# Performance work log

Hardware: AMD Instinct MI355X
Metric: run time of the kernel (lower is better)

Reference implementation:

```python
import jax, jax.numpy as jnp
import numpy as np

N, E = 100000, 1600000
ENT, OCU, SAI, IJ = 64, 64, 64, 8


def setup_inputs() -> dict:
    key = jax.random.key(0)
    ks = jax.random.split(key, 14)

    def lin(k, fan_in, fan_out):
        s = 1.0 / np.sqrt(fan_in)
        kw, kb = jax.random.split(k)
        w = jax.random.uniform(kw, (fan_in, fan_out), minval=-s, maxval=s, dtype=jnp.float32)
        b = jax.random.uniform(kb, (fan_out,), minval=-s, maxval=s, dtype=jnp.float32)
        return w, b

    we_w1, we_b1 = lin(ks[0], 2 * ENT + 1 + IJ, OCU)
    we_w2, we_b2 = lin(ks[1], OCU, OCU)
    wx_w1, wx_b1 = lin(ks[2], OCU, OCU)
    wx_w2, wx_b2 = lin(ks[3], OCU, 1)
    wh_w1, wh_b1 = lin(ks[4], ENT + OCU, OCU)
    wh_w2, wh_b2 = lin(ks[5], OCU, SAI)
    wv_w1, wv_b1 = lin(ks[6], ENT, OCU)
    wv_w2, wv_b2 = lin(ks[7], OCU, 1)

    return {
        "h": jax.random.normal(ks[8], (N, ENT), dtype=jnp.float32),
        "x": jax.random.normal(ks[9], (N, 3), dtype=jnp.float32),
        "velocidade": jax.random.normal(ks[10], (N, 3), dtype=jnp.float32),
        "atributos_arestas": jax.random.normal(ks[11], (E, IJ), dtype=jnp.float32),
        "we_w1": we_w1, "we_b1": we_b1, "we_w2": we_w2, "we_b2": we_b2,
        "wx_w1": wx_w1, "wx_b1": wx_b1, "wx_w2": wx_w2, "wx_b2": wx_b2,
        "wh_w1": wh_w1, "wh_b1": wh_b1, "wh_w2": wh_w2, "wh_b2": wh_b2,
        "wv_w1": wv_w1, "wv_b1": wv_b1, "wv_w2": wv_w2, "wv_b2": wv_b2,
        "arestas": jax.random.randint(ks[12], (2, E), 0, N, dtype=jnp.int32),
    }


def reference(h, x, velocidade, atributos_arestas,
              we_w1, we_b1, we_w2, we_b2,
              wx_w1, wx_b1, wx_w2, wx_b2,
              wh_w1, wh_b1, wh_w2, wh_b2,
              wv_w1, wv_b1, wv_w2, wv_b2,
              arestas):
    linhas, cols = arestas[0], arestas[1]
    n = h.shape[0]

    # gather endpoint coordinates, radial distance per edge
    diferenca = x[linhas] - x[cols]                            # [E, 3]
    dif_radial = jnp.sum(diferenca * diferenca, axis=1, keepdims=True)  # [E, 1]

    # edge MLP phi_e on [h_i, h_j, ||x_i-x_j||^2, edge_attr]
    atributos = jnp.concatenate([h[linhas], h[cols], dif_radial, atributos_arestas], axis=1)
    m_ij = jnp.tanh(jnp.tanh(atributos @ we_w1 + we_b1) @ we_w2 + we_b2)   # [E, OCU]

    # phi_x: per-edge scalar gate on coordinate differences
    phi_x = jnp.tanh(jnp.tanh(m_ij @ wx_w1 + wx_b1) @ wx_w2 + wx_b2)       # [E, 1]

    # phi_v: per-node scalar gate on velocity
    phi_v = jnp.tanh(h @ wv_w1 + wv_b1) @ wv_w2 + wv_b2                    # [N, 1]

    # segment-mean of (diferenca * phi_x) over source nodes
    trans = diferenca * phi_x                                              # [E, 3]
    agg_sum = jax.ops.segment_sum(trans, linhas, num_segments=n)           # [N, 3]
    cnt = jax.ops.segment_sum(jnp.ones((E, 1), trans.dtype), linhas, num_segments=n)
    agg_mean = agg_sum / jnp.maximum(cnt, 1.0)

    velocidade_nova = velocidade * phi_v + agg_mean
    x_nova = x + velocidade_nova

    # segment-sum of edge messages, node update phi_h
    m_i = jax.ops.segment_sum(m_ij, linhas, num_segments=n)                # [N, OCU]
    h_cat = jnp.concatenate([h, m_i], axis=1)
    h_nova = jnp.tanh(h_cat @ wh_w1 + wh_b1) @ wh_w2 + wh_b2               # [N, SAI]

    return (h_nova, x_nova, velocidade_nova)
```

## Files before the change

### kernel.cpp

```cpp
#include <hip/hip_runtime.h>


typedef unsigned int uint;
typedef unsigned short u16;
typedef __attribute__((ext_vector_type(8))) short short8;
typedef __attribute__((ext_vector_type(4))) float f32x4;

#define UB_LO(u) __uint_as_float((u) << 16)
#define UB_HI(u) __uint_as_float((u) & 0xffff0000u)

__device__ __forceinline__ float fast_tanh(float x) {
    float e = __expf(2.0f * x);
    return 1.0f - 2.0f * __builtin_amdgcn_rcpf(e + 1.0f);
}
__device__ __forceinline__ u16 bf16rne(float f) {
    uint u = __float_as_uint(f);
    return (u16)((u + 0x7fffu + ((u >> 16) & 1u)) >> 16);
}
__device__ __forceinline__ uint packbf(float a, float b) {
    return (uint)bf16rne(a) | ((uint)bf16rne(b) << 16);
}
__device__ __forceinline__ uint packbf_fast(float a, float b) {
    return __builtin_amdgcn_perm(__float_as_uint(b), __float_as_uint(a), 0x07060302u);
}
__device__ __forceinline__ u16 trunc16(float f) {
    return (u16)(__float_as_uint(f) >> 16);
}
__device__ __forceinline__ int swzb(int b) { return b ^ ((b >> 3) & 0x70); }

__global__ void wprep_kernel(const float* __restrict__ we_w1, const float* __restrict__ we_w2,
                             const float* __restrict__ wx_w1, const float* __restrict__ wv_w1,
                             const float* __restrict__ wh_w1, const float* __restrict__ wh_w2,
                             u16* __restrict__ we1t, u16* __restrict__ we2t,
                             u16* __restrict__ wx1t, u16* __restrict__ wv1t,
                             u16* __restrict__ wh1t, u16* __restrict__ wh2t,
                             u16* __restrict__ wert) {
    int t = blockIdx.x * 256 + threadIdx.x;
    if (t < 8192) {
        int j = t >> 7, k = t & 127;
        we1t[t] = bf16rne(we_w1[k * 64 + j]);
        wh1t[t] = bf16rne(wh_w1[k * 64 + j]);
    }
    if (t < 4096) {
        int n = t >> 6, k = t & 63;
        we2t[t] = bf16rne(we_w2[k * 64 + n]);
        wx1t[t] = bf16rne(wx_w1[k * 64 + n]);
        wv1t[t] = bf16rne(wv_w1[k * 64 + n]);
        wh2t[t] = bf16rne(wh_w2[k * 64 + n]);
    }
    if (t < 2048) {
        int n = t >> 5, k = t & 31;
        float v = 0.0f;
        if (k == 0) v = we_w1[128 * 64 + n];
        else if (k <= 8) v = we_w1[(128 + k) * 64 + n];
        wert[t] = bf16rne(v);
    }
}

__global__ __launch_bounds__(256, 2)
void pre_mfma_kernel(const float* __restrict__ h, const float* __restrict__ we_b1,
                     const u16* __restrict__ we1t,
                     u16* __restrict__ HrB, u16* __restrict__ HcB, int N)
{
    __shared__ u16 X1[4096];
    __shared__ u16 X2[4096];
    const int tid = threadIdx.x, lane = tid & 63, wv = tid >> 6;
    const int nb = blockIdx.x * 64;
    const int el = tid >> 2, jg = tid & 3;
    const int fn = lane & 15, fk8 = (lane >> 4) * 8;

    {
        uint pk[8];
        if (nb + el < N) {
            const float4* h4 = (const float4*)(h + (size_t)(nb + el) * 64 + jg * 16);
            #pragma unroll
            for (int q = 0; q < 4; q++) {
                float4 v = h4[q];
                pk[2*q]   = packbf_fast(v.x, v.y);
                pk[2*q+1] = packbf_fast(v.z, v.w);
            }
        } else {
            #pragma unroll
            for (int q = 0; q < 8; q++) pk[q] = 0;
        }
        const int b0 = swzb(el * 128 + jg * 32), b1 = swzb(el * 128 + jg * 32 + 16);
        *(uint4*)(&X1[b0 >> 1]) = make_uint4(pk[0], pk[1], pk[2], pk[3]);
        *(uint4*)(&X1[b1 >> 1]) = make_uint4(pk[4], pk[5], pk[6], pk[7]);
    }
    __syncthreads();

    const int mb = wv * 16;
    short8 a0, a1;
    {
        const int ba = swzb((mb + fn) * 128 + fk8 * 2);
        const int bb = swzb((mb + fn) * 128 + 64 + fk8 * 2);
        a0 = *(const short8*)(&X1[ba >> 1]);
        a1 = *(const short8*)(&X1[bb >> 1]);
    }
    #pragma unroll
    for (int n0 = 0; n0 < 4; n0++) {
        uint4 bw0 = *(const uint4*)(we1t + (n0*16 + fn) * 128 + fk8);
        uint4 bw1 = *(const uint4*)(we1t + (n0*16 + fn) * 128 + 32 + fk8);
        const float bias = we_b1[n0 * 16 + fn];
        f32x4 q = {bias, bias, bias, bias};
        q = __builtin_amdgcn_mfma_f32_16x16x32_bf16(a0, __builtin_bit_cast(short8, bw0), q, 0, 0, 0);
        q = __builtin_amdgcn_mfma_f32_16x16x32_bf16(a1, __builtin_bit_cast(short8, bw1), q, 0, 0, 0);
        #pragma unroll
        for (int r2 = 0; r2 < 4; r2++) {
            const int m = mb + (lane >> 4) * 4 + r2;
            X2[swzb(m * 128 + (n0*16 + fn) * 2) >> 1] = bf16rne(q[r2]);
        }
    }
    __syncthreads();
    if (nb + el < N) {
        const int b0 = swzb(el * 128 + jg * 32), b1 = swzb(el * 128 + jg * 32 + 16);
        uint4 v0 = *(const uint4*)(&X2[b0 >> 1]);
        uint4 v1 = *(const uint4*)(&X2[b1 >> 1]);
        u16* o = HrB + (size_t)(nb + el) * 64 + jg * 16;
        *(uint4*)o = v0; *(uint4*)(o + 8) = v1;
    }
    __syncthreads();
    #pragma unroll
    for (int n0 = 0; n0 < 4; n0++) {
        uint4 bw0 = *(const uint4*)(we1t + (n0*16 + fn) * 128 + 64 + fk8);
        uint4 bw1 = *(const uint4*)(we1t + (n0*16 + fn) * 128 + 96 + fk8);
        f32x4 q = {0.f, 0.f, 0.f, 0.f};
        q = __builtin_amdgcn_mfma_f32_16x16x32_bf16(a0, __builtin_bit_cast(short8, bw0), q, 0, 0, 0);
        q = __builtin_amdgcn_mfma_f32_16x16x32_bf16(a1, __builtin_bit_cast(short8, bw1), q, 0, 0, 0);
        #pragma unroll
        for (int r2 = 0; r2 < 4; r2++) {
            const int m = mb + (lane >> 4) * 4 + r2;
            X2[swzb(m * 128 + (n0*16 + fn) * 2) >> 1] = bf16rne(q[r2]);
        }
    }
    __syncthreads();
    if (nb + el < N) {
        const int b0 = swzb(el * 128 + jg * 32), b1 = swzb(el * 128 + jg * 32 + 16);
        uint4 v0 = *(const uint4*)(&X2[b0 >> 1]);
        uint4 v1 = *(const uint4*)(&X2[b1 >> 1]);
        u16* o = HcB + (size_t)(nb + el) * 64 + jg * 16;
        *(uint4*)o = v0; *(uint4*)(o + 8) = v1;
    }
}

__global__ __launch_bounds__(256, 2)
void edge_mfma_kernel(const float* __restrict__ x, const float* __restrict__ eattr,
                      const int* __restrict__ perm, const int* __restrict__ rowp,
                      const int* __restrict__ colp,
                      const u16* __restrict__ HrB, const u16* __restrict__ HcB,
                      const u16* __restrict__ wert,
                      const u16* __restrict__ we2t, const float* __restrict__ we_b2,
                      const u16* __restrict__ wx1t, const float* __restrict__ wx_b1,
                      const float* __restrict__ wx_w2, const float* __restrict__ wx_b2,
                      float* __restrict__ miF, float* __restrict__ aggF,
                      float* __restrict__ cntF, int E)
{
    __shared__ u16 Xp[4096];
    __shared__ u16 X1[4096];
    __shared__ u16 X2[4096];
    __shared__ float dS[64][3];
    __shared__ float pxS[64];
    __shared__ int rS[64];

    const int tid = threadIdx.x, lane = tid & 63, wv = tid >> 6;
    int bid = blockIdx.x;
    const int nwg = gridDim.x;
    if ((nwg & 7) == 0) bid = (bid & 7) * (nwg >> 3) + (bid >> 3);
    const int sb = bid * 64;
    const int fn = lane & 15, fk8 = (lane >> 4) * 8;
    const int el = tid >> 2, jg = tid & 3;
    const int s = sb + el;
    const int mb = wv * 16;

    {
        int r = -1, c = 0;
        if (s < E) { r = rowp[s]; c = colp[s]; }
        if (jg == 0) rS[el] = r;
        uint pk[8];
        if (s < E) {
            if (jg == 0) {
                dS[el][0] = x[(size_t)r*3+0] - x[(size_t)c*3+0];
                dS[el][1] = x[(size_t)r*3+1] - x[(size_t)c*3+1];
                dS[el][2] = x[(size_t)r*3+2] - x[(size_t)c*3+2];
            }
            uint4 ra = *(const uint4*)(HrB + (size_t)r * 64 + jg * 16);
            uint4 rb = *(const uint4*)(HrB + (size_t)r * 64 + jg * 16 + 8);
            uint4 ca = *(const uint4*)(HcB + (size_t)c * 64 + jg * 16);
            uint4 cb = *(const uint4*)(HcB + (size_t)c * 64 + jg * 16 + 8);
            uint rw[8] = {ra.x, ra.y, ra.z, ra.w, rb.x, rb.y, rb.z, rb.w};
            uint cw[8] = {ca.x, ca.y, ca.z, ca.w, cb.x, cb.y, cb.z, cb.w};
            #pragma unroll
            for (int q = 0; q < 8; q++) {
                const float lo = UB_LO(rw[q]) + UB_LO(cw[q]);
                const float hi = UB_HI(rw[q]) + UB_HI(cw[q]);
                pk[q] = packbf_fast(lo, hi);
            }
        } else {
            #pragma unroll
            for (int q = 0; q < 8; q++) pk[q] = 0;
        }
        const int b0 = swzb(el * 128 + jg * 32), b1 = swzb(el * 128 + jg * 32 + 16);
        *(uint4*)(&Xp[b0 >> 1]) = make_uint4(pk[0], pk[1], pk[2], pk[3]);
        *(uint4*)(&Xp[b1 >> 1]) = make_uint4(pk[4], pk[5], pk[6], pk[7]);
    }

    uint ae[4] = {0, 0, 0, 0};
    {
        const int kc = lane >> 4;
        const int s2 = sb + mb + fn;
        if (kc < 2 && s2 < E) {
            const int e2 = perm[s2];
            const float4* ea4 = (const float4*)(eattr + (size_t)e2 * 8);
            float4 u0 = ea4[0], u1 = ea4[1];
            if (kc == 0) {
                const int r2_ = rowp[s2], c2_ = colp[s2];
                const float dd0 = x[(size_t)r2_*3+0] - x[(size_t)c2_*3+0];
                const float dd1 = x[(size_t)r2_*3+1] - x[(size_t)c2_*3+1];
                const float dd2 = x[(size_t)r2_*3+2] - x[(size_t)c2_*3+2];
                const float rad = dd0*dd0 + dd1*dd1 + dd2*dd2;
                ae[0] = packbf_fast(rad,  u0.x);
                ae[1] = packbf_fast(u0.y, u0.z);
                ae[2] = packbf_fast(u0.w, u1.x);
                ae[3] = packbf_fast(u1.y, u1.z);
            } else {
                ae[0] = packbf_fast(u1.w, 0.0f);
            }
        }
    }
    const short8 a_e = __builtin_bit_cast(short8, *(uint4*)ae);
    __syncthreads();

    #pragma unroll
    for (int n0 = 0; n0 < 4; n0++) {
        uint4 bw = *(const uint4*)(wert + (n0*16 + fn) * 32 + fk8);
        f32x4 q = {0.f, 0.f, 0.f, 0.f};
        q = __builtin_amdgcn_mfma_f32_16x16x32_bf16(a_e, __builtin_bit_cast(short8, bw), q, 0, 0, 0);
        #pragma unroll
        for (int r2 = 0; r2 < 4; r2++) {
            const int idx = swzb((mb + (lane >> 4) * 4 + r2) * 128 + (n0*16 + fn) * 2) >> 1;
            const float pre = q[r2] + UB_LO((uint)Xp[idx]);
            X1[idx] = trunc16(fast_tanh(pre));
        }
    }
    __syncthreads();

    short8 a0, a1;
    {
        const int ba = swzb((mb + fn) * 128 + fk8 * 2);
        const int bb = swzb((mb + fn) * 128 + 64 + fk8 * 2);
        a0 = *(const short8*)(&X1[ba >> 1]);
        a1 = *(const short8*)(&X1[bb >> 1]);
    }
    #pragma unroll
    for (int n0 = 0; n0 < 4; n0++) {
        uint4 bw0 = *(const uint4*)(we2t + (n0*16 + fn) * 64 + fk8);
        uint4 bw1 = *(const uint4*)(we2t + (n0*16 + fn) * 64 + 32 + fk8);
        const float bias = we_b2[n0 * 16 + fn];
        f32x4 q = {bias, bias, bias, bias};
        q = __builtin_amdgcn_mfma_f32_16x16x32_bf16(a0, __builtin_bit_cast(short8, bw0), q, 0, 0, 0);
        q = __builtin_amdgcn_mfma_f32_16x16x32_bf16(a1, __builtin_bit_cast(short8, bw1), q, 0, 0, 0);
        #pragma unroll
        for (int r2 = 0; r2 < 4; r2++) {
            const int m = mb + (lane >> 4) * 4 + r2;
            X2[swzb(m * 128 + (n0*16 + fn) * 2) >> 1] = bf16rne(fast_tanh(q[r2]));
        }
    }
    __syncthreads();

    short8 c0, c1;
    {
        const int ba = swzb((mb + fn) * 128 + fk8 * 2);
        const int bb = swzb((mb + fn) * 128 + 64 + fk8 * 2);
        c0 = *(const short8*)(&X2[ba >> 1]);
        c1 = *(const short8*)(&X2[bb >> 1]);
    }
    float pxp[4] = {0.f, 0.f, 0.f, 0.f};
    #pragma unroll
    for (int n0 = 0; n0 < 4; n0++) {
        uint4 bw0 = *(const uint4*)(wx1t + (n0*16 + fn) * 64 + fk8);
        uint4 bw1 = *(const uint4*)(wx1t + (n0*16 + fn) * 64 + 32 + fk8);
        const float bias = wx_b1[n0 * 16 + fn];
        f32x4 q = {bias, bias, bias, bias};
        q = __builtin_amdgcn_mfma_f32_16x16x32_bf16(c0, __builtin_bit_cast(short8, bw0), q, 0, 0, 0);
        q = __builtin_amdgcn_mfma_f32_16x16x32_bf16(c1, __builtin_bit_cast(short8, bw1), q, 0, 0, 0);
        const float wqn = wx_w2[n0 * 16 + fn];
        #pragma unroll
        for (int r2 = 0; r2 < 4; r2++) pxp[r2] += fast_tanh(q[r2]) * wqn;
    }
    #pragma unroll
    for (int off = 1; off < 16; off <<= 1) {
        #pragma unroll
        for (int r2 = 0; r2 < 4; r2++) pxp[r2] += __shfl_xor(pxp[r2], off, 64);
    }
    if (fn == 0) {
        const float bx2 = wx_b2[0];
        #pragma unroll
        for (int r2 = 0; r2 < 4; r2++) {
            const int m = mb + (lane >> 4) * 4 + r2;
            pxS[m] = fast_tanh(pxp[r2] + bx2);
        }
    }
    __syncthreads();

    const int w16 = wv * 16;
    for (int s0 = w16; s0 < w16 + 16; s0++) {
        const int r0 = rS[s0];
        if (r0 < 0) continue;
        if (s0 > 0 && rS[s0 - 1] == r0) continue;
        int s1 = s0 + 1;
        while (s1 < 64 && rS[s1] == r0) s1++;
        float msum = 0.0f, tsum = 0.0f;
        for (int t = s0; t < s1; t++) {
            msum += UB_LO((uint)X2[swzb(t * 128 + lane * 2) >> 1]);
            if (lane < 3) tsum += dS[t][lane] * pxS[t];
        }
        atomicAdd(&miF[(size_t)r0 * 64 + lane], msum);
        if (lane < 3) atomicAdd(&aggF[(size_t)r0 * 3 + lane], tsum);
        if (lane == 3) atomicAdd(&cntF[r0], (float)(s1 - s0));
    }
}

__global__ __launch_bounds__(256, 2)
void aggnode_kernel(const float* __restrict__ h, const float* __restrict__ x,
                    const float* __restrict__ vel,
                    const float* __restrict__ miF, const float* __restrict__ aggF,
                    const float* __restrict__ cntF,
                    const u16* __restrict__ wv1t, const float* __restrict__ wv_b1,
                    const float* __restrict__ wv_w2, const float* __restrict__ wv_b2,
                    const u16* __restrict__ wh1t, const float* __restrict__ wh_b1,
                    const u16* __restrict__ wh2t, const float* __restrict__ wh_b2,
                    float* __restrict__ out_h, float* __restrict__ out_x,
                    float* __restrict__ out_v, int N)
{
    __shared__ u16 Xh[4096];
    __shared__ u16 Xm[4096];
    __shared__ float aggM[64][3];
    __shared__ float pvS[64];

    const int tid = threadIdx.x, lane = tid & 63, wv = tid >> 6;
    const int nb = blockIdx.x * 64;
    const int el = tid >> 2, jg = tid & 3;
    const int fn = lane & 15, fk8 = (lane >> 4) * 8;

    {
        uint pk[8];
        if (nb + el < N) {
            const float4* h4 = (const float4*)(h + (size_t)(nb + el) * 64 + jg * 16);
            #pragma unroll
            for (int q = 0; q < 4; q++) {
                float4 v = h4[q];
                pk[2*q]   = packbf_fast(v.x, v.y);
                pk[2*q+1] = packbf_fast(v.z, v.w);
            }
        } else {
            #pragma unroll
            for (int q = 0; q < 8; q++) pk[q] = 0;
        }
        const int b0 = swzb(el * 128 + jg * 32), b1 = swzb(el * 128 + jg * 32 + 16);
        *(uint4*)(&Xh[b0 >> 1]) = make_uint4(pk[0], pk[1], pk[2], pk[3]);
        *(uint4*)(&Xh[b1 >> 1]) = make_uint4(pk[4], pk[5], pk[6], pk[7]);
    }

    for (int t = 0; t < 16; t++) {
        const int ln = wv * 16 + t;
        const int n = nb + ln;
        float val = 0.0f;
        if (n < N) val = miF[(size_t)n * 64 + lane];
        Xm[swzb(ln * 128 + lane * 2) >> 1] = bf16rne(val);
        if (lane < 3 && n < N) {
            const float cf = cntF[n];
            aggM[ln][lane] = aggF[(size_t)n * 3 + lane] / fmaxf(cf, 1.0f);
        }
    }
    __syncthreads();

    const int mb = wv * 16;
    short8 a0, a1, b0, b1;
    {
        const int ba = swzb((mb + fn) * 128 + fk8 * 2);
        const int bb = swzb((mb + fn) * 128 + 64 + fk8 * 2);
        a0 = *(const short8*)(&Xh[ba >> 1]);
        a1 = *(const short8*)(&Xh[bb >> 1]);
        b0 = *(const short8*)(&Xm[ba >> 1]);
        b1 = *(const short8*)(&Xm[bb >> 1]);
    }

    float pvp[4] = {0.f, 0.f, 0.f, 0.f};
    #pragma unroll
    for (int n0 = 0; n0 < 4; n0++) {
        uint4 bw0 = *(const uint4*)(wv1t + (n0*16 + fn) * 64 + fk8);
        uint4 bw1 = *(const uint4*)(wv1t + (n0*16 + fn) * 64 + 32 + fk8);
        const float bias = wv_b1[n0 * 16 + fn];
        f32x4 q = {bias, bias, bias, bias};
        q = __builtin_amdgcn_mfma_f32_16x16x32_bf16(a0, __builtin_bit_cast(short8, bw0), q, 0, 0, 0);
        q = __builtin_amdgcn_mfma_f32_16x16x32_bf16(a1, __builtin_bit_cast(short8, bw1), q, 0, 0, 0);
        const float wqn = wv_w2[n0 * 16 + fn];
        #pragma unroll
        for (int r2 = 0; r2 < 4; r2++) pvp[r2] += fast_tanh(q[r2]) * wqn;
    }
    #pragma unroll
    for (int off = 1; off < 16; off <<= 1) {
        #pragma unroll
        for (int r2 = 0; r2 < 4; r2++) pvp[r2] += __shfl_xor(pvp[r2], off, 64);
    }
    if (fn == 0) {
        const float bv2 = wv_b2[0];
        #pragma unroll
        for (int r2 = 0; r2 < 4; r2++) pvS[mb + (lane >> 4) * 4 + r2] = pvp[r2] + bv2;
    }
    __syncthreads();

    #pragma unroll
    for (int n0 = 0; n0 < 4; n0++) {
        const u16* base = wh1t + (n0*16 + fn) * 128;
        uint4 bw0 = *(const uint4*)(base + fk8);
        uint4 bw1 = *(const uint4*)(base + 32 + fk8);
        uint4 bw2 = *(const uint4*)(base + 64 + fk8);
        uint4 bw3 = *(const uint4*)(base + 96 + fk8);
        const float bias = wh_b1[n0 * 16 + fn];
        f32x4 q = {bias, bias, bias, bias};
        q = __builtin_amdgcn_mfma_f32_16x16x32_bf16(a0, __builtin_bit_cast(short8, bw0), q, 0, 0, 0);
        q = __builtin_amdgcn_mfma_f32_16x16x32_bf16(a1, __builtin_bit_cast(short8, bw1), q, 0, 0, 0);
        q = __builtin_amdgcn_mfma_f32_16x16x32_bf16(b0, __builtin_bit_cast(short8, bw2), q, 0, 0, 0);
        q = __builtin_amdgcn_mfma_f32_16x16x32_bf16(b1, __builtin_bit_cast(short8, bw3), q, 0, 0, 0);
        #pragma unroll
        for (int r2 = 0; r2 < 4; r2++) {
            const int m = mb + (lane >> 4) * 4 + r2;
            Xm[swzb(m * 128 + (n0*16 + fn) * 2) >> 1] = bf16rne(fast_tanh(q[r2]));
        }
    }
    __syncthreads();

    short8 c0, c1;
    {
        const int ba = swzb((mb + fn) * 128 + fk8 * 2);
        const int bb = swzb((mb + fn) * 128 + 64 + fk8 * 2);
        c0 = *(const short8*)(&Xm[ba >> 1]);
        c1 = *(const short8*)(&Xm[bb >> 1]);
    }
    #pragma unroll
    for (int n0 = 0; n0 < 4; n0++) {
        uint4 bw0 = *(const uint4*)(wh2t + (n0*16 + fn) * 64 + fk8);
        uint4 bw1 = *(const uint4*)(wh2t + (n0*16 + fn) * 64 + 32 + fk8);
        const float bias = wh_b2[n0 * 16 + fn];
        f32x4 q = {bias, bias, bias, bias};
        q = __builtin_amdgcn_mfma_f32_16x16x32_bf16(c0, __builtin_bit_cast(short8, bw0), q, 0, 0, 0);
        q = __builtin_amdgcn_mfma_f32_16x16x32_bf16(c1, __builtin_bit_cast(short8, bw1), q, 0, 0, 0);
        #pragma unroll
        for (int r2 = 0; r2 < 4; r2++) {
            const int m = mb + (lane >> 4) * 4 + r2;
            if (nb + m < N) out_h[(size_t)(nb + m) * 64 + n0 * 16 + fn] = q[r2];
        }
    }

    if (tid < 64 && nb + tid < N) {
        const int n = nb + tid;
        const float pv = pvS[tid];
        #pragma unroll
        for (int d = 0; d < 3; d++) {
            const float am = aggM[tid][d];
            const float vn = vel[(size_t)n * 3 + d] * pv + am;
            out_v[(size_t)n * 3 + d] = vn;
            out_x[(size_t)n * 3 + d] = x[(size_t)n * 3 + d] + vn;
        }
    }
}

__global__ void hist_kernel(const int* __restrict__ rows, int* __restrict__ hist, int E) {
    int e = blockIdx.x * blockDim.x + threadIdx.x;
    if (e < E) atomicAdd(&hist[rows[e]], 1);
}

__global__ __launch_bounds__(256)
void scan1_kernel(const int* __restrict__ hist, int* __restrict__ bsum, int N) {
    const int t = threadIdx.x, b = blockIdx.x;
    const int base = b * 1024 + t * 4;
    int s = 0;
    #pragma unroll
    for (int q = 0; q < 4; q++) s += (base + q < N) ? hist[base + q] : 0;
    #pragma unroll
    for (int off = 1; off < 64; off <<= 1) s += __shfl_xor(s, off, 64);
    __shared__ int ws[4];
    if ((t & 63) == 0) ws[t >> 6] = s;
    __syncthreads();
    if (t == 0) bsum[b] = ws[0] + ws[1] + ws[2] + ws[3];
}

__global__ __launch_bounds__(256)
void scan2_kernel(int* __restrict__ bsum, int nb) {
    __shared__ int buf[1024];
    const int t = threadIdx.x;
    for (int i = t; i < nb; i += 256) buf[i] = bsum[i];
    __syncthreads();
    if (t == 0) {
        int run = 0;
        for (int i = 0; i < nb; i++) { int v = buf[i]; buf[i] = run; run += v; }
    }
    __syncthreads();
    for (int i = t; i < nb; i += 256) bsum[i] = buf[i];
}

__global__ __launch_bounds__(256)
void scan3_kernel(const int* __restrict__ hist, const int* __restrict__ bbase,
                  int* __restrict__ offs, int* __restrict__ cursor, int N) {
    const int t = threadIdx.x, b = blockIdx.x;
    const int base = b * 1024 + t * 4;
    int v[4];
    #pragma unroll
    for (int q = 0; q < 4; q++) v[q] = (base + q < N) ? hist[base + q] : 0;
    const int s = v[0] + v[1] + v[2] + v[3];
    const int lane = t & 63, wid = t >> 6;
    int inc = s;
    #pragma unroll
    for (int off = 1; off < 64; off <<= 1) {
        int u = __shfl_up(inc, off, 64);
        if (lane >= off) inc += u;
    }
    __shared__ int wtot[4];
    if (lane == 63) wtot[wid] = inc;
    __syncthreads();
    int wbase = 0;
    #pragma unroll
    for (int wq = 0; wq < 3; wq++) if (wq < wid) wbase += wtot[wq];
    int run = bbase[b] + wbase + (inc - s);
    #pragma unroll
    for (int q = 0; q < 4; q++) {
        const int i = base + q;
        if (i < N) { cursor[i] = run; run += v[q]; offs[i + 1] = run; }
    }
    if (b == 0 && t == 0) offs[0] = 0;
}

__global__ void scatter_kernel(const int* __restrict__ rows, const int* __restrict__ cols,
                               int* __restrict__ cursor,
                               int* __restrict__ perm, int* __restrict__ colp, int E) {
    int e = blockIdx.x * blockDim.x + threadIdx.x;
    if (e < E) {
        int p = atomicAdd(&cursor[rows[e]], 1);
        perm[p] = e;
        colp[p] = cols[e];
    }
}

__global__ void rowfill_kernel(const int* __restrict__ offs, int* __restrict__ rowp, int N) {
    int n = blockIdx.x * blockDim.x + threadIdx.x;
    if (n < N) {
        const int b = offs[n], e = offs[n + 1];
        for (int i = b; i < e; i++) rowp[i] = n;
    }
}

template<int BLK>
__global__ __launch_bounds__(BLK)
void edge_atomic_kernel(const float* __restrict__ h, const float* __restrict__ x,
                 const float* __restrict__ eattr,
                 const int* __restrict__ rows, const int* __restrict__ cols,
                 const float* __restrict__ we_w1, const float* __restrict__ we_b1,
                 const float* __restrict__ we_w2, const float* __restrict__ we_b2,
                 const float* __restrict__ wx_w1, const float* __restrict__ wx_b1,
                 const float* __restrict__ wx_w2, const float* __restrict__ wx_b2,
                 float* __restrict__ agg, float* __restrict__ cnt, float* __restrict__ mi,
                 int E)
{
    __shared__ float act[64][BLK];
    const int tid = threadIdx.x;
    const int e = blockIdx.x * BLK + tid;
    if (e >= E) return;

    const int r = rows[e];
    const int c = cols[e];
    const float d0 = x[(size_t)r*3+0] - x[(size_t)c*3+0];
    const float d1 = x[(size_t)r*3+1] - x[(size_t)c*3+1];
    const float d2 = x[(size_t)r*3+2] - x[(size_t)c*3+2];
    const float rad = d0*d0 + d1*d1 + d2*d2;

    float A[64];
    #pragma unroll
    for (int j = 0; j < 64; j++) A[j] = we_b1[j];
    const float* hr = h + (size_t)r * 64;
    const float* hc = h + (size_t)c * 64;
    #pragma unroll 4
    for (int k = 0; k < 64; k++) {
        const float a0 = hr[k];
        const float a1 = hc[k];
        const float* w0 = we_w1 + k * 64;
        const float* w1 = we_w1 + (64 + k) * 64;
        #pragma unroll
        for (int j = 0; j < 64; j++) A[j] += a0 * w0[j] + a1 * w1[j];
    }
    {
        const float* w = we_w1 + 128 * 64;
        #pragma unroll
        for (int j = 0; j < 64; j++) A[j] += rad * w[j];
    }
    const float* ea = eattr + (size_t)e * 8;
    #pragma unroll
    for (int k = 0; k < 8; k++) {
        const float a = ea[k];
        const float* w = we_w1 + (129 + k) * 64;
        #pragma unroll
        for (int j = 0; j < 64; j++) A[j] += a * w[j];
    }
    #pragma unroll
    for (int j = 0; j < 64; j++) act[j][tid] = fast_tanh(A[j]);

    float B[64];
    #pragma unroll
    for (int j = 0; j < 64; j++) B[j] = we_b2[j];
    #pragma unroll 4
    for (int k = 0; k < 64; k++) {
        const float a = act[k][tid];
        const float* w = we_w2 + k * 64;
        #pragma unroll
        for (int j = 0; j < 64; j++) B[j] += a * w[j];
    }
    #pragma unroll
    for (int j = 0; j < 64; j++) act[j][tid] = fast_tanh(B[j]);

    #pragma unroll
    for (int j = 0; j < 64; j++) A[j] = wx_b1[j];
    #pragma unroll 4
    for (int k = 0; k < 64; k++) {
        const float a = act[k][tid];
        const float* w = wx_w1 + k * 64;
        #pragma unroll
        for (int j = 0; j < 64; j++) A[j] += a * w[j];
    }
    float px = wx_b2[0];
    #pragma unroll
    for (int j = 0; j < 64; j++) px += fast_tanh(A[j]) * wx_w2[j];
    px = fast_tanh(px);

    atomicAdd(&agg[(size_t)r*3+0], d0 * px);
    atomicAdd(&agg[(size_t)r*3+1], d1 * px);
    atomicAdd(&agg[(size_t)r*3+2], d2 * px);
    atomicAdd(&cnt[r], 1.0f);
    float* mir = mi + (size_t)r * 64;
    #pragma unroll
    for (int j = 0; j < 64; j++) atomicAdd(&mir[j], act[j][tid]);
}

template<int BLK>
__global__ __launch_bounds__(BLK, 2)
void node_fb_kernel(const float* __restrict__ h, const float* __restrict__ x,
                 const float* __restrict__ vel,
                 const float* __restrict__ wh_w1, const float* __restrict__ wh_b1,
                 const float* __restrict__ wh_w2, const float* __restrict__ wh_b2,
                 const float* __restrict__ wv_w1, const float* __restrict__ wv_b1,
                 const float* __restrict__ wv_w2, const float* __restrict__ wv_b2,
                 const float* __restrict__ agg, const float* __restrict__ cnt,
                 const float* __restrict__ mi,
                 float* __restrict__ out_h, float* __restrict__ out_x, float* __restrict__ out_v,
                 int N)
{
    const int n = blockIdx.x * BLK + threadIdx.x;
    if (n >= N) return;

    const float* hn = h + (size_t)n * 64;
    const float* mn = mi + (size_t)n * 64;

    float A[64];
    #pragma unroll
    for (int j = 0; j < 64; j++) A[j] = wv_b1[j];
    #pragma unroll
    for (int k = 0; k < 64; k++) {
        const float a = hn[k];
        const float* w = wv_w1 + k * 64;
        #pragma unroll
        for (int j = 0; j < 64; j++) A[j] += a * w[j];
    }
    float pv = wv_b2[0];
    #pragma unroll
    for (int j = 0; j < 64; j++) pv += fast_tanh(A[j]) * wv_w2[j];

    #pragma unroll
    for (int j = 0; j < 64; j++) A[j] = wh_b1[j];
    #pragma unroll
    for (int k = 0; k < 64; k++) {
        const float a0 = hn[k];
        const float a1 = mn[k];
        const float* w0 = wh_w1 + k * 64;
        const float* w1 = wh_w1 + (64 + k) * 64;
        #pragma unroll
        for (int j = 0; j < 64; j++) A[j] += a0 * w0[j] + a1 * w1[j];
    }
    #pragma unroll
    for (int j = 0; j < 64; j++) A[j] = fast_tanh(A[j]);

    float B[64];
    #pragma unroll
    for (int j = 0; j < 64; j++) B[j] = wh_b2[j];
    #pragma unroll
    for (int k = 0; k < 64; k++) {
        const float a = A[k];
        const float* w = wh_w2 + k * 64;
        #pragma unroll
        for (int j = 0; j < 64; j++) B[j] += a * w[j];
    }
    float* oh = out_h + (size_t)n * 64;
    #pragma unroll
    for (int j = 0; j < 64; j++) oh[j] = B[j];

    const float inv = 1.0f / fmaxf(cnt[n], 1.0f);
    #pragma unroll
    for (int d = 0; d < 3; d++) {
        const float am = agg[(size_t)n*3 + d] * inv;
        const float vn = vel[(size_t)n*3 + d] * pv + am;
        out_v[(size_t)n*3 + d] = vn;
        out_x[(size_t)n*3 + d] = x[(size_t)n*3 + d] + vn;
    }
}

extern "C" void kernel_launch(void* const* d_in, const int* in_sizes, int n_in,
                              void* d_out, int out_size, void* d_ws, size_t ws_size,
                              hipStream_t stream) {
    const float* h      = (const float*)d_in[0];
    const float* x      = (const float*)d_in[1];
    const float* vel    = (const float*)d_in[2];
    const float* eattr  = (const float*)d_in[3];
    const float* we_w1  = (const float*)d_in[4];
    const float* we_b1  = (const float*)d_in[5];
    const float* we_w2  = (const float*)d_in[6];
    const float* we_b2  = (const float*)d_in[7];
    const float* wx_w1  = (const float*)d_in[8];
    const float* wx_b1  = (const float*)d_in[9];
    const float* wx_w2  = (const float*)d_in[10];
    const float* wx_b2  = (const float*)d_in[11];
    const float* wh_w1  = (const float*)d_in[12];
    const float* wh_b1  = (const float*)d_in[13];
    const float* wh_w2  = (const float*)d_in[14];
    const float* wh_b2  = (const float*)d_in[15];
    const float* wv_w1  = (const float*)d_in[16];
    const float* wv_b1  = (const float*)d_in[17];
    const float* wv_w2  = (const float*)d_in[18];
    const float* wv_b2  = (const float*)d_in[19];
    const int*   ar     = (const int*)d_in[20];

    const int N = in_sizes[0] / 64;
    const int E = in_sizes[20] / 2;
    const int* rows = ar;
    const int* cols = ar + E;

    float* out_h = (float*)d_out;
    float* out_x = out_h + (size_t)N * 64;
    float* out_v = out_x + (size_t)N * 3;

    u16* HrB = (u16*)d_out;
    u16* HcB = HrB + (size_t)N * 64;

    const int nbScan = (N + 1023) / 1024;

    char* p = (char*)d_ws;
    float* miF  = (float*)p; p += (size_t)N * 64 * sizeof(float);
    float* aggF = (float*)p; p += (size_t)N * 3 * sizeof(float);
    float* cntF = (float*)p; p += (size_t)N * sizeof(float);
    int*  hist  = (int*)p;   p += (size_t)N * sizeof(int);
    const size_t zero_bytes = (size_t)(p - (char*)d_ws);
    int*  offs  = (int*)p;   p += (size_t)(N + 1) * sizeof(int);
    int*  cursor= (int*)p;   p += (size_t)N * sizeof(int);
    int*  bsum  = (int*)p;   p += (size_t)(nbScan > 0 ? nbScan : 1) * sizeof(int);
    int*  perm  = (int*)p;   p += (size_t)E * sizeof(int);
    int*  rowp  = (int*)p;   p += (size_t)E * sizeof(int);
    int*  colp  = (int*)p;   p += (size_t)E * sizeof(int);
    p = (char*)(((uintptr_t)p + 63) & ~(uintptr_t)63);
    u16*  we1t = (u16*)p;   p += 64 * 128 * sizeof(u16);
    u16*  we2t = (u16*)p;   p += 64 * 64 * sizeof(u16);
    u16*  wx1t = (u16*)p;   p += 64 * 64 * sizeof(u16);
    u16*  wv1t = (u16*)p;   p += 64 * 64 * sizeof(u16);
    u16*  wh1t = (u16*)p;   p += 64 * 128 * sizeof(u16);
    u16*  wh2t = (u16*)p;   p += 64 * 64 * sizeof(u16);
    u16*  wert = (u16*)p;   p += 64 * 32 * sizeof(u16);
    const size_t needed = (size_t)(p - (char*)d_ws);

    if (ws_size >= needed && nbScan <= 1024) {
        hipMemsetAsync(d_ws, 0, zero_bytes, stream);
        hist_kernel<<<(E + 255) / 256, 256, 0, stream>>>(rows, hist, E);
        scan1_kernel<<<nbScan, 256, 0, stream>>>(hist, bsum, N);
        scan2_kernel<<<1, 256, 0, stream>>>(bsum, nbScan);
        scan3_kernel<<<nbScan, 256, 0, stream>>>(hist, bsum, offs, cursor, N);
        scatter_kernel<<<(E + 255) / 256, 256, 0, stream>>>(rows, cols, cursor, perm, colp, E);
        rowfill_kernel<<<(N + 255) / 256, 256, 0, stream>>>(offs, rowp, N);

        wprep_kernel<<<32, 256, 0, stream>>>(we_w1, we_w2, wx_w1, wv_w1, wh_w1, wh_w2,
                                             we1t, we2t, wx1t, wv1t, wh1t, wh2t, wert);
        pre_mfma_kernel<<<(N + 63) / 64, 256, 0, stream>>>(h, we_b1, we1t, HrB, HcB, N);

        edge_mfma_kernel<<<(E + 63) / 64, 256, 0, stream>>>(
            x, eattr, perm, rowp, colp, HrB, HcB,
            wert, we2t, we_b2, wx1t, wx_b1, wx_w2, wx_b2,
            miF, aggF, cntF, E);

        aggnode_kernel<<<(N + 63) / 64, 256, 0, stream>>>(
            h, x, vel, miF, aggF, cntF,
            wv1t, wv_b1, wv_w2, wv_b2,
            wh1t, wh_b1, wh2t, wh_b2,
            out_h, out_x, out_v, N);
    } else {
        float* agg2 = (float*)d_ws;
        float* cnt2 = agg2 + (size_t)N * 3;
        float* mi2  = cnt2 + N;
        hipMemsetAsync(d_ws, 0, (size_t)N * 68 * sizeof(float), stream);

        edge_atomic_kernel<128><<<(E + 127) / 128, 128, 0, stream>>>(
            h, x, eattr, rows, cols,
            we_w1, we_b1, we_w2, we_b2,
            wx_w1, wx_b1, wx_w2, wx_b2,
            agg2, cnt2, mi2, E);

        node_fb_kernel<128><<<(N + 127) / 128, 128, 0, stream>>>(
            h, x, vel,
            wh_w1, wh_b1, wh_w2, wh_b2,
            wv_w1, wv_b1, wv_w2, wv_b2,
            agg2, cnt2, mi2, out_h, out_x, out_v, N);
    }
}
```

Before: 578.7 us.

## Share one LDS tile in edge kernel, pack row/col pairs, drop rowfill

Merges the three per-stage LDS tiles of the edge kernel into one buffer that is overwritten in place, removing two block barriers. The launch-bounds occupancy hint rises from 2 to 8 blocks per CU. Row and column indices are now stored as a single int2 array written by the scatter kernel, so the separate rowfill kernel goes away. The squared radial distance is computed once and shared through LDS instead of being recomputed with extra x gathers. The tighter occupancy hint caps registers per thread and may cause spills, and in-place reuse of the tile relies on each wave touching only its own rows.

```diff
diff --git a/kernel.cpp b/kernel.cpp
--- a/kernel.cpp
+++ b/kernel.cpp
@@ -143,10 +143,9 @@
     }
 }
 
-__global__ __launch_bounds__(256, 2)
+__global__ __launch_bounds__(256, 8)
 void edge_mfma_kernel(const float* __restrict__ x, const float* __restrict__ eattr,
-                      const int* __restrict__ perm, const int* __restrict__ rowp,
-                      const int* __restrict__ colp,
+                      const int* __restrict__ perm, const int2* __restrict__ rc,
                       const u16* __restrict__ HrB, const u16* __restrict__ HcB,
                       const u16* __restrict__ wert,
                       const u16* __restrict__ we2t, const float* __restrict__ we_b2,
@@ -155,11 +154,10 @@
                       float* __restrict__ miF, float* __restrict__ aggF,
                       float* __restrict__ cntF, int E)
 {
-    __shared__ u16 Xp[4096];
-    __shared__ u16 X1[4096];
-    __shared__ u16 X2[4096];
+    __shared__ u16 T[4096];
     __shared__ float dS[64][3];
     __shared__ float pxS[64];
+    __shared__ float radS[64];
     __shared__ int rS[64];
 
     const int tid = threadIdx.x, lane = tid & 63, wv = tid >> 6;
@@ -174,14 +172,16 @@
 
     {
         int r = -1, c = 0;
-        if (s < E) { r = rowp[s]; c = colp[s]; }
+        if (s < E) { int2 p2 = rc[s]; r = p2.x; c = p2.y; }
         if (jg == 0) rS[el] = r;
         uint pk[8];
         if (s < E) {
             if (jg == 0) {
-                dS[el][0] = x[(size_t)r*3+0] - x[(size_t)c*3+0];
-                dS[el][1] = x[(size_t)r*3+1] - x[(size_t)c*3+1];
-                dS[el][2] = x[(size_t)r*3+2] - x[(size_t)c*3+2];
+                const float d0 = x[(size_t)r*3+0] - x[(size_t)c*3+0];
+                const float d1 = x[(size_t)r*3+1] - x[(size_t)c*3+1];
+                const float d2 = x[(size_t)r*3+2] - x[(size_t)c*3+2];
+                dS[el][0] = d0; dS[el][1] = d1; dS[el][2] = d2;
+                radS[el] = d0*d0 + d1*d1 + d2*d2;
             }
             uint4 ra = *(const uint4*)(HrB + (size_t)r * 64 + jg * 16);
             uint4 rb = *(const uint4*)(HrB + (size_t)r * 64 + jg * 16 + 8);
@@ -200,9 +200,10 @@
             for (int q = 0; q < 8; q++) pk[q] = 0;
         }
         const int b0 = swzb(el * 128 + jg * 32), b1 = swzb(el * 128 + jg * 32 + 16);
-        *(uint4*)(&Xp[b0 >> 1]) = make_uint4(pk[0], pk[1], pk[2], pk[3]);
-        *(uint4*)(&Xp[b1 >> 1]) = make_uint4(pk[4], pk[5], pk[6], pk[7]);
-    }
+        *(uint4*)(&T[b0 >> 1]) = make_uint4(pk[0], pk[1], pk[2], pk[3]);
+        *(uint4*)(&T[b1 >> 1]) = make_uint4(pk[4], pk[5], pk[6], pk[7]);
+    }
+    __syncthreads();
 
     uint ae[4] = {0, 0, 0, 0};
     {
@@ -211,24 +212,20 @@
         if (kc < 2 && s2 < E) {
             const int e2 = perm[s2];
             const float4* ea4 = (const float4*)(eattr + (size_t)e2 * 8);
-            float4 u0 = ea4[0], u1 = ea4[1];
             if (kc == 0) {
-                const int r2_ = rowp[s2], c2_ = colp[s2];
-                const float dd0 = x[(size_t)r2_*3+0] - x[(size_t)c2_*3+0];
-                const float dd1 = x[(size_t)r2_*3+1] - x[(size_t)c2_*3+1];
-                const float dd2 = x[(size_t)r2_*3+2] - x[(size_t)c2_*3+2];
-                const float rad = dd0*dd0 + dd1*dd1 + dd2*dd2;
+                float4 u0 = ea4[0], u1 = ea4[1];
+                const float rad = radS[mb + fn];
                 ae[0] = packbf_fast(rad,  u0.x);
                 ae[1] = packbf_fast(u0.y, u0.z);
                 ae[2] = packbf_fast(u0.w, u1.x);
                 ae[3] = packbf_fast(u1.y, u1.z);
             } else {
+                float4 u1 = ea4[1];
                 ae[0] = packbf_fast(u1.w, 0.0f);
             }
         }
     }
     const short8 a_e = __builtin_bit_cast(short8, *(uint4*)ae);
-    __syncthreads();
 
     #pragma unroll
     for (int n0 = 0; n0 < 4; n0++) {
@@ -238,18 +235,17 @@
         #pragma unroll
         for (int r2 = 0; r2 < 4; r2++) {
             const int idx = swzb((mb + (lane >> 4) * 4 + r2) * 128 + (n0*16 + fn) * 2) >> 1;
-            const float pre = q[r2] + UB_LO((uint)Xp[idx]);
-            X1[idx] = trunc16(fast_tanh(pre));
-        }
-    }
-    __syncthreads();
+            const float pre = q[r2] + UB_LO((uint)T[idx]);
+            T[idx] = trunc16(fast_tanh(pre));
+        }
+    }
 
     short8 a0, a1;
     {
         const int ba = swzb((mb + fn) * 128 + fk8 * 2);
         const int bb = swzb((mb + fn) * 128 + 64 + fk8 * 2);
-        a0 = *(const short8*)(&X1[ba >> 1]);
-        a1 = *(const short8*)(&X1[bb >> 1]);
+        a0 = *(const short8*)(&T[ba >> 1]);
+        a1 = *(const short8*)(&T[bb >> 1]);
     }
     #pragma unroll
     for (int n0 = 0; n0 < 4; n0++) {
@@ -262,17 +258,16 @@
         #pragma unroll
         for (int r2 = 0; r2 < 4; r2++) {
             const int m = mb + (lane >> 4) * 4 + r2;
-            X2[swzb(m * 128 + (n0*16 + fn) * 2) >> 1] = bf16rne(fast_tanh(q[r2]));
-        }
-    }
-    __syncthreads();
+            T[swzb(m * 128 + (n0*16 + fn) * 2) >> 1] = bf16rne(fast_tanh(q[r2]));
+        }
+    }
 
     short8 c0, c1;
     {
         const int ba = swzb((mb + fn) * 128 + fk8 * 2);
         const int bb = swzb((mb + fn) * 128 + 64 + fk8 * 2);
-        c0 = *(const short8*)(&X2[ba >> 1]);
-        c1 = *(const short8*)(&X2[bb >> 1]);
+        c0 = *(const short8*)(&T[ba >> 1]);
+        c1 = *(const short8*)(&T[bb >> 1]);
     }
     float pxp[4] = {0.f, 0.f, 0.f, 0.f};
     #pragma unroll
@@ -311,7 +306,7 @@
         while (s1 < 64 && rS[s1] == r0) s1++;
         float msum = 0.0f, tsum = 0.0f;
         for (int t = s0; t < s1; t++) {
-            msum += UB_LO((uint)X2[swzb(t * 128 + lane * 2) >> 1]);
+            msum += UB_LO((uint)T[swzb(t * 128 + lane * 2) >> 1]);
             if (lane < 3) tsum += dS[t][lane] * pxS[t];
         }
         atomicAdd(&miF[(size_t)r0 * 64 + lane], msum);
@@ -533,20 +528,13 @@
 
 __global__ void scatter_kernel(const int* __restrict__ rows, const int* __restrict__ cols,
                                int* __restrict__ cursor,
-                               int* __restrict__ perm, int* __restrict__ colp, int E) {
+                               int* __restrict__ perm, int2* __restrict__ rc, int E) {
     int e = blockIdx.x * blockDim.x + threadIdx.x;
     if (e < E) {
-        int p = atomicAdd(&cursor[rows[e]], 1);
+        int r = rows[e];
+        int p = atomicAdd(&cursor[r], 1);
         perm[p] = e;
-        colp[p] = cols[e];
-    }
-}
-
-__global__ void rowfill_kernel(const int* __restrict__ offs, int* __restrict__ rowp, int N) {
-    int n = blockIdx.x * blockDim.x + threadIdx.x;
-    if (n < N) {
-        const int b = offs[n], e = offs[n + 1];
-        for (int i = b; i < e; i++) rowp[i] = n;
+        rc[p] = make_int2(r, cols[e]);
     }
 }
 
@@ -760,8 +748,8 @@
     int*  cursor= (int*)p;   p += (size_t)N * sizeof(int);
     int*  bsum  = (int*)p;   p += (size_t)(nbScan > 0 ? nbScan : 1) * sizeof(int);
     int*  perm  = (int*)p;   p += (size_t)E * sizeof(int);
-    int*  rowp  = (int*)p;   p += (size_t)E * sizeof(int);
-    int*  colp  = (int*)p;   p += (size_t)E * sizeof(int);
+    p = (char*)(((uintptr_t)p + 7) & ~(uintptr_t)7);
+    int2* rc    = (int2*)p;  p += (size_t)E * sizeof(int2);
     p = (char*)(((uintptr_t)p + 63) & ~(uintptr_t)63);
     u16*  we1t = (u16*)p;   p += 64 * 128 * sizeof(u16);
     u16*  we2t = (u16*)p;   p += 64 * 64 * sizeof(u16);
@@ -778,15 +766,14 @@
         scan1_kernel<<<nbScan, 256, 0, stream>>>(hist, bsum, N);
         scan2_kernel<<<1, 256, 0, stream>>>(bsum, nbScan);
         scan3_kernel<<<nbScan, 256, 0, stream>>>(hist, bsum, offs, cursor, N);
-        scatter_kernel<<<(E + 255) / 256, 256, 0, stream>>>(rows, cols, cursor, perm, colp, E);
-        rowfill_kernel<<<(N + 255) / 256, 256, 0, stream>>>(offs, rowp, N);
+        scatter_kernel<<<(E + 255) / 256, 256, 0, stream>>>(rows, cols, cursor, perm, rc, E);
 
         wprep_kernel<<<32, 256, 0, stream>>>(we_w1, we_w2, wx_w1, wv_w1, wh_w1, wh_w2,
                                              we1t, we2t, wx1t, wv1t, wh1t, wh2t, wert);
         pre_mfma_kernel<<<(N + 63) / 64, 256, 0, stream>>>(h, we_b1, we1t, HrB, HcB, N);
 
         edge_mfma_kernel<<<(E + 63) / 64, 256, 0, stream>>>(
-            x, eattr, perm, rowp, colp, HrB, HcB,
+            x, eattr, perm, rc, HrB, HcB,
             wert, we2t, we_b2, wx1t, wx_b1, wx_w2, wx_b2,
             miF, aggF, cntF, E);
 
```

Result: faster. 552.0 us (-4.6%).
